# Optimization experiments

Measured on AMD Instinct MI355X. Metric: run time of the kernel, lower is better.

The kernel has to match this reference:

```python
import jax, jax.numpy as jnp
import numpy as np

D_MODEL = 1024
N_HEADS = 16
D_K = D_MODEL // N_HEADS


def setup_inputs() -> dict:
    key = jax.random.key(0)
    ks = jax.random.split(key, 11)
    B, S = 2, 2048
    s = 1.0 / np.sqrt(D_MODEL)
    return {
        "Q": jax.random.normal(ks[0], (B, S, D_MODEL), jnp.float32),
        "K": jax.random.normal(ks[1], (B, S, D_MODEL), jnp.float32),
        "V": jax.random.normal(ks[2], (B, S, D_MODEL), jnp.float32),
        "Wq": jax.random.normal(ks[3], (D_MODEL, D_MODEL), jnp.float32) * s,
        "bq": jnp.zeros((D_MODEL,), jnp.float32),
        "Wk": jax.random.normal(ks[4], (D_MODEL, D_MODEL), jnp.float32) * s,
        "bk": jnp.zeros((D_MODEL,), jnp.float32),
        "Wv": jax.random.normal(ks[5], (D_MODEL, D_MODEL), jnp.float32) * s,
        "bv": jnp.zeros((D_MODEL,), jnp.float32),
        "Wo": jax.random.normal(ks[6], (D_MODEL, D_MODEL), jnp.float32) * s,
        "bo": jnp.zeros((D_MODEL,), jnp.float32),
    }


def reference(Q, K, V, Wq, bq, Wk, bk, Wv, bv, Wo, bo):
    B, S, _ = Q.shape
    # linear projections (torch Linear: x @ W.T + b), split into heads
    def proj(x, W, b):
        y = x @ W.T + b                          # [B,S,D]
        return y.reshape(B, -1, N_HEADS, D_K).transpose(0, 2, 1, 3)  # [B,H,S,d_k]
    q = proj(Q, Wq, bq)
    k = proj(K, Wk, bk)
    v = proj(V, Wv, bv)
    scale = 1.0 / jnp.sqrt(jnp.float32(D_K))
    scores = jnp.einsum('bhqd,bhkd->bhqk', q, k) * scale  # [B,H,S,S]
    attn = jax.nn.softmax(scores, axis=-1)
    out = jnp.einsum('bhqk,bhkd->bhqd', attn, v)          # [B,H,S,d_k]
    out = out.transpose(0, 2, 1, 3).reshape(B, S, N_HEADS * D_K)
    return out @ Wo.T + bo
```

## Files before the change

### kernel.cpp

```cpp
#include <hip/hip_runtime.h>
#include <hip/hip_bf16.h>
#include <math.h>

#define D_MODEL 1024
#define NH      16
#define DK      64
#define S_LEN   2048
#define BATCH   2
#define M_ROWS  4096

typedef _Float16 f16;
typedef _Float16 f16x8 __attribute__((ext_vector_type(8)));
typedef float    f32x4 __attribute__((ext_vector_type(4)));

__device__ __forceinline__ float exp2_fast(float x) {
    float r;
    asm("v_exp_f32 %0, %1" : "=v"(r) : "v"(x));
    return r;
}

__device__ __forceinline__ int perm6(int k) {
    return (k & 35) | ((k & 12) << 1) | ((k & 16) >> 2);
}

__global__ __launch_bounds__(256) void cvt_f32_to_f16(
    const float* __restrict__ a, const float* __restrict__ b,
    const float* __restrict__ c, const float* __restrict__ d,
    f16* __restrict__ oa, f16* __restrict__ ob,
    f16* __restrict__ oc, f16* __restrict__ od, int n8) {
    const int y = blockIdx.y;
    const float* s = (y == 0) ? a : (y == 1) ? b : (y == 2) ? c : d;
    f16* o        = (y == 0) ? oa : (y == 1) ? ob : (y == 2) ? oc : od;
    if (s == nullptr) return;
    const int i = blockIdx.x * 256 + threadIdx.x;
    if (i >= n8) return;
    const size_t e = (size_t)i * 8;
    const float4 v0 = *(const float4*)&s[e];
    const float4 v1 = *(const float4*)&s[e + 4];
    f16x8 r = {(f16)v0.x, (f16)v0.y, (f16)v0.z, (f16)v0.w,
               (f16)v1.x, (f16)v1.y, (f16)v1.z, (f16)v1.w};
    *(f16x8*)&o[e] = r;
}

__device__ __forceinline__ void stage16(const f16* g, f16* l) {
    __builtin_amdgcn_global_load_lds(
        (const __attribute__((address_space(1))) unsigned int*)g,
        (__attribute__((address_space(3))) unsigned int*)l, 16, 0, 0);
}

__device__ __forceinline__ void gemm_body(f16* As, f16* Bs,
                                          const f16* __restrict__ X, const f16* __restrict__ W,
                                          const float* __restrict__ bias, void* __restrict__ Yv,
                                          const int mode, const float oscale) {
    const int tid = threadIdx.x;
    const int lane = tid & 63;
    const int w  = tid >> 6;
    const int wm = w >> 1, wn = w & 1;
    const int l15 = lane & 15, lhi = lane >> 4;
    const int m0 = blockIdx.y * 128, n0 = blockIdx.x * 128;

    const int srow = tid >> 2;
    const int scol = (tid & 3) * 8;

    f32x4 acc[4][4] = {};

    for (int k0 = 0; k0 < D_MODEL; k0 += 32) {
        __syncthreads();
        stage16(&X[(size_t)(m0 + srow) * D_MODEL + k0 + scol],      &As[tid * 8]);
        stage16(&X[(size_t)(m0 + 64 + srow) * D_MODEL + k0 + scol], &As[2048 + tid * 8]);
        stage16(&W[(size_t)(n0 + srow) * D_MODEL + k0 + scol],      &Bs[tid * 8]);
        stage16(&W[(size_t)(n0 + 64 + srow) * D_MODEL + k0 + scol], &Bs[2048 + tid * 8]);
        __syncthreads();
        f16x8 af[4], bf[4];
#pragma unroll
        for (int mt = 0; mt < 4; ++mt) af[mt] = *(const f16x8*)&As[(wm * 64 + mt * 16 + l15) * 32 + lhi * 8];
#pragma unroll
        for (int nt = 0; nt < 4; ++nt) bf[nt] = *(const f16x8*)&Bs[(wn * 64 + nt * 16 + l15) * 32 + lhi * 8];
#pragma unroll
        for (int mt = 0; mt < 4; ++mt)
#pragma unroll
            for (int nt = 0; nt < 4; ++nt)
                acc[mt][nt] = __builtin_amdgcn_mfma_f32_16x16x32_f16(af[mt], bf[nt], acc[mt][nt], 0, 0, 0);
    }

#pragma unroll
    for (int mt = 0; mt < 4; ++mt)
#pragma unroll
        for (int nt = 0; nt < 4; ++nt) {
            const int n = n0 + wn * 64 + nt * 16 + l15;
            const float bn = bias[n];
#pragma unroll
            for (int r = 0; r < 4; ++r) {
                const int m = m0 + wm * 64 + mt * 16 + lhi * 4 + r;
                const float v = (acc[mt][nt][r] + bn) * oscale;
                if (mode == 0) {
                    ((f16*)Yv)[((((size_t)(m >> 11) * NH + (n >> 6)) * S_LEN) + (m & 2047)) * DK + (n & 63)] = (f16)v;
                } else {
                    ((float*)Yv)[(size_t)m * D_MODEL + n] = v;
                }
            }
        }
}

__device__ __forceinline__ void gemm_body_vswap(f16* As, f16* Bs,
                                                const f16* __restrict__ X, const f16* __restrict__ W,
                                                const float* __restrict__ bias, f16* __restrict__ vt) {
    const int tid = threadIdx.x;
    const int lane = tid & 63;
    const int w  = tid >> 6;
    const int wm = w >> 1, wn = w & 1;
    const int l15 = lane & 15, lhi = lane >> 4;
    const int m0 = blockIdx.y * 128, n0 = blockIdx.x * 128;

    const int srow = tid >> 2;
    const int scol = (tid & 3) * 8;

    f32x4 acc[4][4] = {};

    for (int k0 = 0; k0 < D_MODEL; k0 += 32) {
        __syncthreads();
        stage16(&X[(size_t)(m0 + srow) * D_MODEL + k0 + scol],      &As[tid * 8]);
        stage16(&X[(size_t)(m0 + 64 + srow) * D_MODEL + k0 + scol], &As[2048 + tid * 8]);
        stage16(&W[(size_t)(n0 + srow) * D_MODEL + k0 + scol],      &Bs[tid * 8]);
        stage16(&W[(size_t)(n0 + 64 + srow) * D_MODEL + k0 + scol], &Bs[2048 + tid * 8]);
        __syncthreads();
        f16x8 af[4], bf[4];
#pragma unroll
        for (int at = 0; at < 4; ++at) af[at] = *(const f16x8*)&Bs[(wm * 64 + at * 16 + l15) * 32 + lhi * 8];
#pragma unroll
        for (int bt = 0; bt < 4; ++bt) bf[bt] = *(const f16x8*)&As[(wn * 64 + bt * 16 + l15) * 32 + lhi * 8];
#pragma unroll
        for (int at = 0; at < 4; ++at)
#pragma unroll
            for (int bt = 0; bt < 4; ++bt)
                acc[at][bt] = __builtin_amdgcn_mfma_f32_16x16x32_f16(af[at], bf[bt], acc[at][bt], 0, 0, 0);
    }

#pragma unroll
    for (int at = 0; at < 4; ++at)
#pragma unroll
        for (int bt = 0; bt < 4; ++bt) {
            const int m = m0 + wn * 64 + bt * 16 + l15;
            const int b = m >> 11, s = m & 2047;
#pragma unroll
            for (int r = 0; r < 4; ++r) {
                const int n = n0 + wm * 64 + at * 16 + lhi * 4 + r;
                const float v = acc[at][bt][r] + bias[n];
                const int s2 = (s & ~63) | perm6(s & 63);
                vt[(((size_t)b * NH + (n >> 6)) * DK + (n & 63)) * S_LEN + s2] = (f16)v;
            }
        }
}

__global__ __launch_bounds__(256) void qkv_gemm(
    const f16* __restrict__ Xq, const f16* __restrict__ Xk, const f16* __restrict__ Xv,
    const f16* __restrict__ Wq, const f16* __restrict__ Wk, const f16* __restrict__ Wv,
    const float* __restrict__ bq, const float* __restrict__ bk, const float* __restrict__ bv,
    f16* __restrict__ qh, f16* __restrict__ kh, f16* __restrict__ vt) {
    __shared__ f16 As[128 * 32];
    __shared__ f16 Bs[128 * 32];
    const int z = blockIdx.z;
    if (z == 2) {
        gemm_body_vswap(As, Bs, Xv, Wv, bv, vt);
    } else if (z == 0) {
        gemm_body(As, Bs, Xq, Wq, bq, qh, 0, 0.125f * 1.44269504f);
    } else {
        gemm_body(As, Bs, Xk, Wk, bk, kh, 0, 1.0f);
    }
}

__global__ __launch_bounds__(256) void out_gemm(const f16* __restrict__ X, const f16* __restrict__ W,
                                                const float* __restrict__ bias, float* __restrict__ Y) {
    __shared__ f16 As[64 * 32];
    __shared__ f16 Bs[128 * 32];
    const int tid = threadIdx.x;
    const int lane = tid & 63;
    const int w  = tid >> 6;
    const int l15 = lane & 15, lhi = lane >> 4;
    const int m0 = blockIdx.y * 64, n0 = blockIdx.x * 128;

    const int srow = tid >> 2;
    const int scol = (tid & 3) * 8;

    f32x4 acc[4][2] = {};

    for (int k0 = 0; k0 < D_MODEL; k0 += 32) {
        __syncthreads();
        stage16(&X[(size_t)(m0 + srow) * D_MODEL + k0 + scol],      &As[tid * 8]);
        stage16(&W[(size_t)(n0 + srow) * D_MODEL + k0 + scol],      &Bs[tid * 8]);
        stage16(&W[(size_t)(n0 + 64 + srow) * D_MODEL + k0 + scol], &Bs[2048 + tid * 8]);
        __syncthreads();
        f16x8 af[4], bf[2];
#pragma unroll
        for (int mt = 0; mt < 4; ++mt) af[mt] = *(const f16x8*)&As[(mt * 16 + l15) * 32 + lhi * 8];
#pragma unroll
        for (int nt = 0; nt < 2; ++nt) bf[nt] = *(const f16x8*)&Bs[(w * 32 + nt * 16 + l15) * 32 + lhi * 8];
#pragma unroll
        for (int mt = 0; mt < 4; ++mt)
#pragma unroll
            for (int nt = 0; nt < 2; ++nt)
                acc[mt][nt] = __builtin_amdgcn_mfma_f32_16x16x32_f16(af[mt], bf[nt], acc[mt][nt], 0, 0, 0);
    }

#pragma unroll
    for (int mt = 0; mt < 4; ++mt)
#pragma unroll
        for (int nt = 0; nt < 2; ++nt) {
            const int n = n0 + w * 32 + nt * 16 + l15;
            const float bn = bias[n];
#pragma unroll
            for (int r = 0; r < 4; ++r) {
                const int m = m0 + mt * 16 + lhi * 4 + r;
                Y[(size_t)m * D_MODEL + n] = acc[mt][nt][r] + bn;
            }
        }
}

__global__ __launch_bounds__(256) void flash_mfma(const f16* __restrict__ qh, const f16* __restrict__ kh,
                                                  const f16* __restrict__ vt, f16* __restrict__ ao) {
    __shared__ f16 Ks[64][72];
    __shared__ f16 Vs[64][72];

    const int tid = threadIdx.x;
    const int lane = tid & 63;
    const int w = tid >> 6;
    const int c = lane & 15;
    const int g = lane >> 4;
    const int qt = blockIdx.x, bh = blockIdx.y;
    const int b = bh >> 4, h = bh & 15;
    const int qrow0 = qt * 64 + w * 16;

    f16x8 bQ0, bQ1;
    {
        const f16* qp = qh + ((size_t)bh * S_LEN + qrow0 + c) * DK;
        bQ0 = *(const f16x8*)&qp[g * 8];
        bQ1 = *(const f16x8*)&qp[32 + g * 8];
    }

    f32x4 oa[4] = {};
    float m_run = -INFINITY;
    float l_run = 0.f;

    const int cr = tid >> 3;
    const int cs = (tid & 7) * 8;

    const f16* kbase = kh + (size_t)bh * S_LEN * DK;
    const f16* vbase = vt + (size_t)bh * DK * S_LEN;

    uint4 kA = *(const uint4*)&kbase[(size_t)(cr) * DK + cs];
    uint4 kB = *(const uint4*)&kbase[(size_t)(cr + 32) * DK + cs];
    uint4 vA = *(const uint4*)&vbase[(size_t)cr * S_LEN + cs];
    uint4 vB = *(const uint4*)&vbase[(size_t)(cr + 32) * S_LEN + cs];

    for (int kt = 0; kt < S_LEN / 64; ++kt) {
        __syncthreads();
        *(uint4*)&Ks[cr][cs]      = kA;
        *(uint4*)&Ks[cr + 32][cs] = kB;
        *(uint4*)&Vs[cr][cs]      = vA;
        *(uint4*)&Vs[cr + 32][cs] = vB;
        if (kt + 1 < S_LEN / 64) {
            const int o = (kt + 1) * 64;
            kA = *(const uint4*)&kbase[(size_t)(o + cr) * DK + cs];
            kB = *(const uint4*)&kbase[(size_t)(o + cr + 32) * DK + cs];
            vA = *(const uint4*)&vbase[(size_t)cr * S_LEN + o + cs];
            vB = *(const uint4*)&vbase[(size_t)(cr + 32) * S_LEN + o + cs];
        }
        __syncthreads();

        f32x4 sc[4] = {};
        __builtin_amdgcn_s_setprio(1);
#pragma unroll
        for (int nt = 0; nt < 4; ++nt) {
            const f16x8 ka = *(const f16x8*)&Ks[nt * 16 + c][g * 8];
            const f16x8 kb = *(const f16x8*)&Ks[nt * 16 + c][32 + g * 8];
            sc[nt] = __builtin_amdgcn_mfma_f32_16x16x32_f16(ka, bQ0, sc[nt], 0, 0, 0);
            sc[nt] = __builtin_amdgcn_mfma_f32_16x16x32_f16(kb, bQ1, sc[nt], 0, 0, 0);
        }
        __builtin_amdgcn_s_setprio(0);

        float tmax = sc[0][0];
#pragma unroll
        for (int nt = 0; nt < 4; ++nt)
#pragma unroll
            for (int r = 0; r < 4; ++r) tmax = fmaxf(tmax, sc[nt][r]);
        tmax = fmaxf(tmax, __shfl_xor(tmax, 16));
        tmax = fmaxf(tmax, __shfl_xor(tmax, 32));

        if (!__all(tmax <= m_run + 8.f)) {
            const float mnew = fmaxf(m_run, tmax);
            const float fac = exp2_fast(m_run - mnew);
            m_run = mnew;
            l_run *= fac;
#pragma unroll
            for (int r = 0; r < 4; ++r) {
                const float fr = __shfl(fac, (lane & 48) + ((lane >> 4) & 3) * 4 + r);
                oa[0][r] *= fr; oa[1][r] *= fr; oa[2][r] *= fr; oa[3][r] *= fr;
            }
        }

        float e[4][4];
        float tsum = 0.f;
#pragma unroll
        for (int nt = 0; nt < 4; ++nt)
#pragma unroll
            for (int r = 0; r < 4; ++r) {
                e[nt][r] = exp2_fast(sc[nt][r] - m_run);
                tsum += e[nt][r];
            }
        tsum += __shfl_xor(tsum, 16);
        tsum += __shfl_xor(tsum, 32);
        l_run += tsum;

        const f16x8 aP0 = {(f16)e[0][0], (f16)e[0][1], (f16)e[0][2], (f16)e[0][3],
                           (f16)e[1][0], (f16)e[1][1], (f16)e[1][2], (f16)e[1][3]};
        const f16x8 aP1 = {(f16)e[2][0], (f16)e[2][1], (f16)e[2][2], (f16)e[2][3],
                           (f16)e[3][0], (f16)e[3][1], (f16)e[3][2], (f16)e[3][3]};

        __builtin_amdgcn_s_setprio(1);
#pragma unroll
        for (int nt2 = 0; nt2 < 4; ++nt2) {
            const f16x8 b0 = *(const f16x8*)&Vs[nt2 * 16 + c][g * 8];
            const f16x8 b1 = *(const f16x8*)&Vs[nt2 * 16 + c][32 + g * 8];
            oa[nt2] = __builtin_amdgcn_mfma_f32_16x16x32_f16(aP0, b0, oa[nt2], 0, 0, 0);
            oa[nt2] = __builtin_amdgcn_mfma_f32_16x16x32_f16(aP1, b1, oa[nt2], 0, 0, 0);
        }
        __builtin_amdgcn_s_setprio(0);
    }

    const float invc = 1.f / l_run;
#pragma unroll
    for (int r = 0; r < 4; ++r) {
        const float ir = __shfl(invc, (lane & 48) + ((lane >> 4) & 3) * 4 + r);
        const int srow = qrow0 + ((lane >> 4) & 3) * 4 + r;
#pragma unroll
        for (int nt2 = 0; nt2 < 4; ++nt2) {
            ao[((size_t)b * S_LEN + srow) * D_MODEL + h * DK + nt2 * 16 + c] = (f16)(oa[nt2][r] * ir);
        }
    }
}

extern "C" void kernel_launch(void* const* d_in, const int* in_sizes, int n_in,
                              void* d_out, int out_size, void* d_ws, size_t ws_size,
                              hipStream_t stream) {
    const float* Q  = (const float*)d_in[0];
    const float* K  = (const float*)d_in[1];
    const float* V  = (const float*)d_in[2];
    const float* Wq = (const float*)d_in[3];
    const float* bq = (const float*)d_in[4];
    const float* Wk = (const float*)d_in[5];
    const float* bk = (const float*)d_in[6];
    const float* Wv = (const float*)d_in[7];
    const float* bv = (const float*)d_in[8];
    const float* Wo = (const float*)d_in[9];
    const float* bo = (const float*)d_in[10];
    float* out = (float*)d_out;

    const size_t NELEM = (size_t)M_ROWS * D_MODEL;
    const size_t WELEM = (size_t)D_MODEL * D_MODEL;
    f16* Qf  = (f16*)d_ws;
    f16* Kf  = Qf + NELEM;
    f16* Vf  = Kf + NELEM;
    f16* Wqf = Vf + NELEM;
    f16* Wkf = Wqf + WELEM;
    f16* Wvf = Wkf + WELEM;
    f16* Wof = Wvf + WELEM;
    f16* qh  = Wof + WELEM;
    f16* kh  = qh + NELEM;
    f16* vtw = kh + NELEM;
    f16* aow = vtw + NELEM;

    cvt_f32_to_f16<<<dim3(2048, 3), 256, 0, stream>>>(Q, K, V, nullptr, Qf, Kf, Vf, nullptr,
                                                      (int)(NELEM / 8));
    cvt_f32_to_f16<<<dim3(512, 4), 256, 0, stream>>>(Wq, Wk, Wv, Wo, Wqf, Wkf, Wvf, Wof,
                                                     (int)(WELEM / 8));
    qkv_gemm<<<dim3(D_MODEL / 128, M_ROWS / 128, 3), 256, 0, stream>>>(
        Qf, Kf, Vf, Wqf, Wkf, Wvf, bq, bk, bv, qh, kh, vtw);
    flash_mfma<<<dim3(S_LEN / 64, BATCH * NH), 256, 0, stream>>>(qh, kh, vtw, aow);
    out_gemm<<<dim3(D_MODEL / 128, M_ROWS / 64), 256, 0, stream>>>(aow, Wof, bo, out);
}
```

Before: 251.5 us.

## Load K/V fragments directly into registers and process two query subtiles per wave

```diff
diff --git a/kernel.cpp b/kernel.cpp
--- a/kernel.cpp
+++ b/kernel.cpp
@@ -218,123 +218,130 @@
 
 __global__ __launch_bounds__(256) void flash_mfma(const f16* __restrict__ qh, const f16* __restrict__ kh,
                                                   const f16* __restrict__ vt, f16* __restrict__ ao) {
-    __shared__ f16 Ks[64][72];
-    __shared__ f16 Vs[64][72];
-
     const int tid = threadIdx.x;
     const int lane = tid & 63;
     const int w = tid >> 6;
-    const int c = lane & 15;
-    const int g = lane >> 4;
-    const int qt = blockIdx.x, bh = blockIdx.y;
+    const int c = lane & 15, g = lane >> 4;
+    const int bid = blockIdx.x;
+    const int swz = (bid & 7) * 64 + (bid >> 3);
+    const int bh = swz >> 4, qt = swz & 15;
     const int b = bh >> 4, h = bh & 15;
-    const int qrow0 = qt * 64 + w * 16;
-
-    f16x8 bQ0, bQ1;
-    {
-        const f16* qp = qh + ((size_t)bh * S_LEN + qrow0 + c) * DK;
-        bQ0 = *(const f16x8*)&qp[g * 8];
-        bQ1 = *(const f16x8*)&qp[32 + g * 8];
-    }
-
-    f32x4 oa[4] = {};
-    float m_run = -INFINITY;
-    float l_run = 0.f;
-
-    const int cr = tid >> 3;
-    const int cs = (tid & 7) * 8;
+    const int qbase = qt * 128 + w * 32;
 
     const f16* kbase = kh + (size_t)bh * S_LEN * DK;
     const f16* vbase = vt + (size_t)bh * DK * S_LEN;
 
-    uint4 kA = *(const uint4*)&kbase[(size_t)(cr) * DK + cs];
-    uint4 kB = *(const uint4*)&kbase[(size_t)(cr + 32) * DK + cs];
-    uint4 vA = *(const uint4*)&vbase[(size_t)cr * S_LEN + cs];
-    uint4 vB = *(const uint4*)&vbase[(size_t)(cr + 32) * S_LEN + cs];
+    f16x8 bQ[2][2];
+#pragma unroll
+    for (int s = 0; s < 2; ++s) {
+        const f16* qp = qh + ((size_t)bh * S_LEN + qbase + s * 16 + c) * DK;
+        bQ[s][0] = *(const f16x8*)&qp[g * 8];
+        bQ[s][1] = *(const f16x8*)&qp[32 + g * 8];
+    }
+
+    f32x4 oa[2][4] = {};
+    float m_run[2] = {-INFINITY, -INFINITY};
+    float l_run[2] = {0.f, 0.f};
+
+    f16x8 kf[8];
+#pragma unroll
+    for (int nt = 0; nt < 4; ++nt) {
+        const f16* kp = &kbase[(size_t)(nt * 16 + c) * DK];
+        kf[nt * 2]     = *(const f16x8*)&kp[g * 8];
+        kf[nt * 2 + 1] = *(const f16x8*)&kp[32 + g * 8];
+    }
 
     for (int kt = 0; kt < S_LEN / 64; ++kt) {
-        __syncthreads();
-        *(uint4*)&Ks[cr][cs]      = kA;
-        *(uint4*)&Ks[cr + 32][cs] = kB;
-        *(uint4*)&Vs[cr][cs]      = vA;
-        *(uint4*)&Vs[cr + 32][cs] = vB;
+        f16x8 vf[8];
+#pragma unroll
+        for (int nt2 = 0; nt2 < 4; ++nt2) {
+            const f16* vp = &vbase[(size_t)(nt2 * 16 + c) * S_LEN + kt * 64];
+            vf[nt2 * 2]     = *(const f16x8*)&vp[g * 8];
+            vf[nt2 * 2 + 1] = *(const f16x8*)&vp[32 + g * 8];
+        }
+
+        f32x4 sc[2][4] = {};
+        __builtin_amdgcn_s_setprio(1);
+#pragma unroll
+        for (int nt = 0; nt < 4; ++nt) {
+#pragma unroll
+            for (int s = 0; s < 2; ++s) {
+                sc[s][nt] = __builtin_amdgcn_mfma_f32_16x16x32_f16(kf[nt * 2],     bQ[s][0], sc[s][nt], 0, 0, 0);
+                sc[s][nt] = __builtin_amdgcn_mfma_f32_16x16x32_f16(kf[nt * 2 + 1], bQ[s][1], sc[s][nt], 0, 0, 0);
+            }
+        }
+        __builtin_amdgcn_s_setprio(0);
+
         if (kt + 1 < S_LEN / 64) {
-            const int o = (kt + 1) * 64;
-            kA = *(const uint4*)&kbase[(size_t)(o + cr) * DK + cs];
-            kB = *(const uint4*)&kbase[(size_t)(o + cr + 32) * DK + cs];
-            vA = *(const uint4*)&vbase[(size_t)cr * S_LEN + o + cs];
-            vB = *(const uint4*)&vbase[(size_t)(cr + 32) * S_LEN + o + cs];
-        }
-        __syncthreads();
-
-        f32x4 sc[4] = {};
-        __builtin_amdgcn_s_setprio(1);
-#pragma unroll
-        for (int nt = 0; nt < 4; ++nt) {
-            const f16x8 ka = *(const f16x8*)&Ks[nt * 16 + c][g * 8];
-            const f16x8 kb = *(const f16x8*)&Ks[nt * 16 + c][32 + g * 8];
-            sc[nt] = __builtin_amdgcn_mfma_f32_16x16x32_f16(ka, bQ0, sc[nt], 0, 0, 0);
-            sc[nt] = __builtin_amdgcn_mfma_f32_16x16x32_f16(kb, bQ1, sc[nt], 0, 0, 0);
-        }
-        __builtin_amdgcn_s_setprio(0);
-
-        float tmax = sc[0][0];
-#pragma unroll
-        for (int nt = 0; nt < 4; ++nt)
-#pragma unroll
-            for (int r = 0; r < 4; ++r) tmax = fmaxf(tmax, sc[nt][r]);
-        tmax = fmaxf(tmax, __shfl_xor(tmax, 16));
-        tmax = fmaxf(tmax, __shfl_xor(tmax, 32));
-
-        if (!__all(tmax <= m_run + 8.f)) {
-            const float mnew = fmaxf(m_run, tmax);
-            const float fac = exp2_fast(m_run - mnew);
-            m_run = mnew;
-            l_run *= fac;
-#pragma unroll
-            for (int r = 0; r < 4; ++r) {
-                const float fr = __shfl(fac, (lane & 48) + ((lane >> 4) & 3) * 4 + r);
-                oa[0][r] *= fr; oa[1][r] *= fr; oa[2][r] *= fr; oa[3][r] *= fr;
-            }
-        }
-
-        float e[4][4];
-        float tsum = 0.f;
-#pragma unroll
-        for (int nt = 0; nt < 4; ++nt)
-#pragma unroll
-            for (int r = 0; r < 4; ++r) {
-                e[nt][r] = exp2_fast(sc[nt][r] - m_run);
-                tsum += e[nt][r];
-            }
-        tsum += __shfl_xor(tsum, 16);
-        tsum += __shfl_xor(tsum, 32);
-        l_run += tsum;
-
-        const f16x8 aP0 = {(f16)e[0][0], (f16)e[0][1], (f16)e[0][2], (f16)e[0][3],
-                           (f16)e[1][0], (f16)e[1][1], (f16)e[1][2], (f16)e[1][3]};
-        const f16x8 aP1 = {(f16)e[2][0], (f16)e[2][1], (f16)e[2][2], (f16)e[2][3],
-                           (f16)e[3][0], (f16)e[3][1], (f16)e[3][2], (f16)e[3][3]};
-
-        __builtin_amdgcn_s_setprio(1);
-#pragma unroll
-        for (int nt2 = 0; nt2 < 4; ++nt2) {
-            const f16x8 b0 = *(const f16x8*)&Vs[nt2 * 16 + c][g * 8];
-            const f16x8 b1 = *(const f16x8*)&Vs[nt2 * 16 + c][32 + g * 8];
-            oa[nt2] = __builtin_amdgcn_mfma_f32_16x16x32_f16(aP0, b0, oa[nt2], 0, 0, 0);
-            oa[nt2] = __builtin_amdgcn_mfma_f32_16x16x32_f16(aP1, b1, oa[nt2], 0, 0, 0);
-        }
-        __builtin_amdgcn_s_setprio(0);
-    }
-
-    const float invc = 1.f / l_run;
-#pragma unroll
-    for (int r = 0; r < 4; ++r) {
-        const float ir = __shfl(invc, (lane & 48) + ((lane >> 4) & 3) * 4 + r);
-        const int srow = qrow0 + ((lane >> 4) & 3) * 4 + r;
-#pragma unroll
-        for (int nt2 = 0; nt2 < 4; ++nt2) {
-            ao[((size_t)b * S_LEN + srow) * D_MODEL + h * DK + nt2 * 16 + c] = (f16)(oa[nt2][r] * ir);
+#pragma unroll
+            for (int nt = 0; nt < 4; ++nt) {
+                const f16* kp = &kbase[(size_t)((kt + 1) * 64 + nt * 16 + c) * DK];
+                kf[nt * 2]     = *(const f16x8*)&kp[g * 8];
+                kf[nt * 2 + 1] = *(const f16x8*)&kp[32 + g * 8];
+            }
+        }
+
+#pragma unroll
+        for (int s = 0; s < 2; ++s) {
+            float tmax = sc[s][0][0];
+#pragma unroll
+            for (int nt = 0; nt < 4; ++nt)
+#pragma unroll
+                for (int r = 0; r < 4; ++r) tmax = fmaxf(tmax, sc[s][nt][r]);
+            tmax = fmaxf(tmax, __shfl_xor(tmax, 16));
+            tmax = fmaxf(tmax, __shfl_xor(tmax, 32));
+
+            if (!__all(tmax <= m_run[s] + 8.f)) {
+                const float mnew = fmaxf(m_run[s], tmax);
+                const float fac = exp2_fast(m_run[s] - mnew);
+                m_run[s] = mnew;
+                l_run[s] *= fac;
+#pragma unroll
+                for (int r = 0; r < 4; ++r) {
+                    const float fr = __shfl(fac, (lane & 48) + ((lane >> 4) & 3) * 4 + r);
+                    oa[s][0][r] *= fr; oa[s][1][r] *= fr; oa[s][2][r] *= fr; oa[s][3][r] *= fr;
+                }
+            }
+
+            float e[4][4];
+            float tsum = 0.f;
+#pragma unroll
+            for (int nt = 0; nt < 4; ++nt)
+#pragma unroll
+                for (int r = 0; r < 4; ++r) {
+                    e[nt][r] = exp2_fast(sc[s][nt][r] - m_run[s]);
+                    tsum += e[nt][r];
+                }
+            tsum += __shfl_xor(tsum, 16);
+            tsum += __shfl_xor(tsum, 32);
+            l_run[s] += tsum;
+
+            const f16x8 aP0 = {(f16)e[0][0], (f16)e[0][1], (f16)e[0][2], (f16)e[0][3],
+                               (f16)e[1][0], (f16)e[1][1], (f16)e[1][2], (f16)e[1][3]};
+            const f16x8 aP1 = {(f16)e[2][0], (f16)e[2][1], (f16)e[2][2], (f16)e[2][3],
+                               (f16)e[3][0], (f16)e[3][1], (f16)e[3][2], (f16)e[3][3]};
+
+            __builtin_amdgcn_s_setprio(1);
+#pragma unroll
+            for (int nt2 = 0; nt2 < 4; ++nt2) {
+                oa[s][nt2] = __builtin_amdgcn_mfma_f32_16x16x32_f16(aP0, vf[nt2 * 2],     oa[s][nt2], 0, 0, 0);
+                oa[s][nt2] = __builtin_amdgcn_mfma_f32_16x16x32_f16(aP1, vf[nt2 * 2 + 1], oa[s][nt2], 0, 0, 0);
+            }
+            __builtin_amdgcn_s_setprio(0);
+        }
+    }
+
+#pragma unroll
+    for (int s = 0; s < 2; ++s) {
+        const float invc = 1.f / l_run[s];
+#pragma unroll
+        for (int r = 0; r < 4; ++r) {
+            const float ir = __shfl(invc, (lane & 48) + ((lane >> 4) & 3) * 4 + r);
+            const int srow = qbase + s * 16 + g * 4 + r;
+#pragma unroll
+            for (int nt2 = 0; nt2 < 4; ++nt2) {
+                ao[((size_t)b * S_LEN + srow) * D_MODEL + h * DK + nt2 * 16 + c] = (f16)(oa[s][nt2][r] * ir);
+            }
         }
     }
 }
@@ -375,6 +382,6 @@
                                                      (int)(WELEM / 8));
     qkv_gemm<<<dim3(D_MODEL / 128, M_ROWS / 128, 3), 256, 0, stream>>>(
         Qf, Kf, Vf, Wqf, Wkf, Wvf, bq, bk, bv, qh, kh, vtw);
-    flash_mfma<<<dim3(S_LEN / 64, BATCH * NH), 256, 0, stream>>>(qh, kh, vtw, aow);
+    flash_mfma<<<512, 256, 0, stream>>>(qh, kh, vtw, aow);
     out_gemm<<<dim3(D_MODEL / 128, M_ROWS / 64), 256, 0, stream>>>(aow, Wof, bo, out);
 }
```

After: 304.9 us. 21.2% more time.

## Merge conversion launches and stage two K/V tiles per barrier in flash kernel

Applied to the files above, without the earlier changes.

```diff
diff --git a/kernel.cpp b/kernel.cpp
--- a/kernel.cpp
+++ b/kernel.cpp
@@ -23,15 +23,19 @@
     return (k & 35) | ((k & 12) << 1) | ((k & 16) >> 2);
 }
 
-__global__ __launch_bounds__(256) void cvt_f32_to_f16(
-    const float* __restrict__ a, const float* __restrict__ b,
-    const float* __restrict__ c, const float* __restrict__ d,
-    f16* __restrict__ oa, f16* __restrict__ ob,
-    f16* __restrict__ oc, f16* __restrict__ od, int n8) {
+__global__ __launch_bounds__(256) void cvt7(
+    const float* __restrict__ s0, const float* __restrict__ s1, const float* __restrict__ s2,
+    const float* __restrict__ s3, const float* __restrict__ s4, const float* __restrict__ s5,
+    const float* __restrict__ s6,
+    f16* __restrict__ d0, f16* __restrict__ d1, f16* __restrict__ d2,
+    f16* __restrict__ d3, f16* __restrict__ d4, f16* __restrict__ d5,
+    f16* __restrict__ d6, int n8big, int n8small) {
     const int y = blockIdx.y;
-    const float* s = (y == 0) ? a : (y == 1) ? b : (y == 2) ? c : d;
-    f16* o        = (y == 0) ? oa : (y == 1) ? ob : (y == 2) ? oc : od;
-    if (s == nullptr) return;
+    const float* s = (y == 0) ? s0 : (y == 1) ? s1 : (y == 2) ? s2 : (y == 3) ? s3
+                   : (y == 4) ? s4 : (y == 5) ? s5 : s6;
+    f16* d        = (y == 0) ? d0 : (y == 1) ? d1 : (y == 2) ? d2 : (y == 3) ? d3
+                   : (y == 4) ? d4 : (y == 5) ? d5 : d6;
+    const int n8 = (y < 3) ? n8big : n8small;
     const int i = blockIdx.x * 256 + threadIdx.x;
     if (i >= n8) return;
     const size_t e = (size_t)i * 8;
@@ -39,7 +43,7 @@
     const float4 v1 = *(const float4*)&s[e + 4];
     f16x8 r = {(f16)v0.x, (f16)v0.y, (f16)v0.z, (f16)v0.w,
                (f16)v1.x, (f16)v1.y, (f16)v1.z, (f16)v1.w};
-    *(f16x8*)&o[e] = r;
+    *(f16x8*)&d[e] = r;
 }
 
 __device__ __forceinline__ void stage16(const f16* g, f16* l) {
@@ -218,8 +222,8 @@
 
 __global__ __launch_bounds__(256) void flash_mfma(const f16* __restrict__ qh, const f16* __restrict__ kh,
                                                   const f16* __restrict__ vt, f16* __restrict__ ao) {
-    __shared__ f16 Ks[64][72];
-    __shared__ f16 Vs[64][72];
+    __shared__ f16 Ks[2][64][72];
+    __shared__ f16 Vs[2][64][72];
 
     const int tid = threadIdx.x;
     const int lane = tid & 63;
@@ -247,84 +251,97 @@
     const f16* kbase = kh + (size_t)bh * S_LEN * DK;
     const f16* vbase = vt + (size_t)bh * DK * S_LEN;
 
-    uint4 kA = *(const uint4*)&kbase[(size_t)(cr) * DK + cs];
-    uint4 kB = *(const uint4*)&kbase[(size_t)(cr + 32) * DK + cs];
-    uint4 vA = *(const uint4*)&vbase[(size_t)cr * S_LEN + cs];
-    uint4 vB = *(const uint4*)&vbase[(size_t)(cr + 32) * S_LEN + cs];
-
-    for (int kt = 0; kt < S_LEN / 64; ++kt) {
-        __syncthreads();
-        *(uint4*)&Ks[cr][cs]      = kA;
-        *(uint4*)&Ks[cr + 32][cs] = kB;
-        *(uint4*)&Vs[cr][cs]      = vA;
-        *(uint4*)&Vs[cr + 32][cs] = vB;
-        if (kt + 1 < S_LEN / 64) {
-            const int o = (kt + 1) * 64;
-            kA = *(const uint4*)&kbase[(size_t)(o + cr) * DK + cs];
-            kB = *(const uint4*)&kbase[(size_t)(o + cr + 32) * DK + cs];
-            vA = *(const uint4*)&vbase[(size_t)cr * S_LEN + o + cs];
-            vB = *(const uint4*)&vbase[(size_t)(cr + 32) * S_LEN + o + cs];
-        }
-        __syncthreads();
-
-        f32x4 sc[4] = {};
-        __builtin_amdgcn_s_setprio(1);
-#pragma unroll
-        for (int nt = 0; nt < 4; ++nt) {
-            const f16x8 ka = *(const f16x8*)&Ks[nt * 16 + c][g * 8];
-            const f16x8 kb = *(const f16x8*)&Ks[nt * 16 + c][32 + g * 8];
-            sc[nt] = __builtin_amdgcn_mfma_f32_16x16x32_f16(ka, bQ0, sc[nt], 0, 0, 0);
-            sc[nt] = __builtin_amdgcn_mfma_f32_16x16x32_f16(kb, bQ1, sc[nt], 0, 0, 0);
-        }
-        __builtin_amdgcn_s_setprio(0);
-
-        float tmax = sc[0][0];
-#pragma unroll
-        for (int nt = 0; nt < 4; ++nt)
-#pragma unroll
-            for (int r = 0; r < 4; ++r) tmax = fmaxf(tmax, sc[nt][r]);
-        tmax = fmaxf(tmax, __shfl_xor(tmax, 16));
-        tmax = fmaxf(tmax, __shfl_xor(tmax, 32));
-
-        if (!__all(tmax <= m_run + 8.f)) {
-            const float mnew = fmaxf(m_run, tmax);
-            const float fac = exp2_fast(m_run - mnew);
-            m_run = mnew;
-            l_run *= fac;
-#pragma unroll
-            for (int r = 0; r < 4; ++r) {
-                const float fr = __shfl(fac, (lane & 48) + ((lane >> 4) & 3) * 4 + r);
-                oa[0][r] *= fr; oa[1][r] *= fr; oa[2][r] *= fr; oa[3][r] *= fr;
-            }
-        }
-
-        float e[4][4];
-        float tsum = 0.f;
-#pragma unroll
-        for (int nt = 0; nt < 4; ++nt)
-#pragma unroll
-            for (int r = 0; r < 4; ++r) {
-                e[nt][r] = exp2_fast(sc[nt][r] - m_run);
-                tsum += e[nt][r];
-            }
-        tsum += __shfl_xor(tsum, 16);
-        tsum += __shfl_xor(tsum, 32);
-        l_run += tsum;
-
-        const f16x8 aP0 = {(f16)e[0][0], (f16)e[0][1], (f16)e[0][2], (f16)e[0][3],
-                           (f16)e[1][0], (f16)e[1][1], (f16)e[1][2], (f16)e[1][3]};
-        const f16x8 aP1 = {(f16)e[2][0], (f16)e[2][1], (f16)e[2][2], (f16)e[2][3],
-                           (f16)e[3][0], (f16)e[3][1], (f16)e[3][2], (f16)e[3][3]};
-
-        __builtin_amdgcn_s_setprio(1);
-#pragma unroll
-        for (int nt2 = 0; nt2 < 4; ++nt2) {
-            const f16x8 b0 = *(const f16x8*)&Vs[nt2 * 16 + c][g * 8];
-            const f16x8 b1 = *(const f16x8*)&Vs[nt2 * 16 + c][32 + g * 8];
-            oa[nt2] = __builtin_amdgcn_mfma_f32_16x16x32_f16(aP0, b0, oa[nt2], 0, 0, 0);
-            oa[nt2] = __builtin_amdgcn_mfma_f32_16x16x32_f16(aP1, b1, oa[nt2], 0, 0, 0);
-        }
-        __builtin_amdgcn_s_setprio(0);
+    uint4 kr[2][2], vr[2][2];
+#pragma unroll
+    for (int s = 0; s < 2; ++s) {
+        kr[s][0] = *(const uint4*)&kbase[(size_t)(s * 64 + cr) * DK + cs];
+        kr[s][1] = *(const uint4*)&kbase[(size_t)(s * 64 + cr + 32) * DK + cs];
+        vr[s][0] = *(const uint4*)&vbase[(size_t)cr * S_LEN + s * 64 + cs];
+        vr[s][1] = *(const uint4*)&vbase[(size_t)(cr + 32) * S_LEN + s * 64 + cs];
+    }
+
+    for (int bt = 0; bt < S_LEN / 128; ++bt) {
+        __syncthreads();
+#pragma unroll
+        for (int s = 0; s < 2; ++s) {
+            *(uint4*)&Ks[s][cr][cs]      = kr[s][0];
+            *(uint4*)&Ks[s][cr + 32][cs] = kr[s][1];
+            *(uint4*)&Vs[s][cr][cs]      = vr[s][0];
+            *(uint4*)&Vs[s][cr + 32][cs] = vr[s][1];
+        }
+        if (bt + 1 < S_LEN / 128) {
+            const int o = (bt + 1) * 128;
+#pragma unroll
+            for (int s = 0; s < 2; ++s) {
+                kr[s][0] = *(const uint4*)&kbase[(size_t)(o + s * 64 + cr) * DK + cs];
+                kr[s][1] = *(const uint4*)&kbase[(size_t)(o + s * 64 + cr + 32) * DK + cs];
+                vr[s][0] = *(const uint4*)&vbase[(size_t)cr * S_LEN + o + s * 64 + cs];
+                vr[s][1] = *(const uint4*)&vbase[(size_t)(cr + 32) * S_LEN + o + s * 64 + cs];
+            }
+        }
+        __syncthreads();
+
+#pragma unroll
+        for (int sub = 0; sub < 2; ++sub) {
+            f32x4 sc[4] = {};
+            __builtin_amdgcn_s_setprio(1);
+#pragma unroll
+            for (int nt = 0; nt < 4; ++nt) {
+                const f16x8 ka = *(const f16x8*)&Ks[sub][nt * 16 + c][g * 8];
+                const f16x8 kb = *(const f16x8*)&Ks[sub][nt * 16 + c][32 + g * 8];
+                sc[nt] = __builtin_amdgcn_mfma_f32_16x16x32_f16(ka, bQ0, sc[nt], 0, 0, 0);
+                sc[nt] = __builtin_amdgcn_mfma_f32_16x16x32_f16(kb, bQ1, sc[nt], 0, 0, 0);
+            }
+            __builtin_amdgcn_s_setprio(0);
+
+            float tmax = sc[0][0];
+#pragma unroll
+            for (int nt = 0; nt < 4; ++nt)
+#pragma unroll
+                for (int r = 0; r < 4; ++r) tmax = fmaxf(tmax, sc[nt][r]);
+            tmax = fmaxf(tmax, __shfl_xor(tmax, 16));
+            tmax = fmaxf(tmax, __shfl_xor(tmax, 32));
+
+            if (!__all(tmax <= m_run + 8.f)) {
+                const float mnew = fmaxf(m_run, tmax);
+                const float fac = exp2_fast(m_run - mnew);
+                m_run = mnew;
+                l_run *= fac;
+#pragma unroll
+                for (int r = 0; r < 4; ++r) {
+                    const float fr = __shfl(fac, (lane & 48) + ((lane >> 4) & 3) * 4 + r);
+                    oa[0][r] *= fr; oa[1][r] *= fr; oa[2][r] *= fr; oa[3][r] *= fr;
+                }
+            }
+
+            float e[4][4];
+            float tsum = 0.f;
+#pragma unroll
+            for (int nt = 0; nt < 4; ++nt)
+#pragma unroll
+                for (int r = 0; r < 4; ++r) {
+                    e[nt][r] = exp2_fast(sc[nt][r] - m_run);
+                    tsum += e[nt][r];
+                }
+            tsum += __shfl_xor(tsum, 16);
+            tsum += __shfl_xor(tsum, 32);
+            l_run += tsum;
+
+            const f16x8 aP0 = {(f16)e[0][0], (f16)e[0][1], (f16)e[0][2], (f16)e[0][3],
+                               (f16)e[1][0], (f16)e[1][1], (f16)e[1][2], (f16)e[1][3]};
+            const f16x8 aP1 = {(f16)e[2][0], (f16)e[2][1], (f16)e[2][2], (f16)e[2][3],
+                               (f16)e[3][0], (f16)e[3][1], (f16)e[3][2], (f16)e[3][3]};
+
+            __builtin_amdgcn_s_setprio(1);
+#pragma unroll
+            for (int nt2 = 0; nt2 < 4; ++nt2) {
+                const f16x8 b0 = *(const f16x8*)&Vs[sub][nt2 * 16 + c][g * 8];
+                const f16x8 b1 = *(const f16x8*)&Vs[sub][nt2 * 16 + c][32 + g * 8];
+                oa[nt2] = __builtin_amdgcn_mfma_f32_16x16x32_f16(aP0, b0, oa[nt2], 0, 0, 0);
+                oa[nt2] = __builtin_amdgcn_mfma_f32_16x16x32_f16(aP1, b1, oa[nt2], 0, 0, 0);
+            }
+            __builtin_amdgcn_s_setprio(0);
+        }
     }
 
     const float invc = 1.f / l_run;
@@ -369,10 +386,9 @@
     f16* vtw = kh + NELEM;
     f16* aow = vtw + NELEM;
 
-    cvt_f32_to_f16<<<dim3(2048, 3), 256, 0, stream>>>(Q, K, V, nullptr, Qf, Kf, Vf, nullptr,
-                                                      (int)(NELEM / 8));
-    cvt_f32_to_f16<<<dim3(512, 4), 256, 0, stream>>>(Wq, Wk, Wv, Wo, Wqf, Wkf, Wvf, Wof,
-                                                     (int)(WELEM / 8));
+    cvt7<<<dim3(2048, 7), 256, 0, stream>>>(Q, K, V, Wq, Wk, Wv, Wo,
+                                            Qf, Kf, Vf, Wqf, Wkf, Wvf, Wof,
+                                            (int)(NELEM / 8), (int)(WELEM / 8));
     qkv_gemm<<<dim3(D_MODEL / 128, M_ROWS / 128, 3), 256, 0, stream>>>(
         Qf, Kf, Vf, Wqf, Wkf, Wvf, bq, bk, bv, qh, kh, vtw);
     flash_mfma<<<dim3(S_LEN / 64, BATCH * NH), 256, 0, stream>>>(qh, kh, vtw, aow);
```

After: 347.9 us. 38.3% more time.

## Stage QKV GEMM epilogue through LDS for coalesced stores; merge conversion launches

Applied to the files above, without the earlier changes.

```diff
diff --git a/kernel.cpp b/kernel.cpp
--- a/kernel.cpp
+++ b/kernel.cpp
@@ -23,15 +23,19 @@
     return (k & 35) | ((k & 12) << 1) | ((k & 16) >> 2);
 }
 
-__global__ __launch_bounds__(256) void cvt_f32_to_f16(
-    const float* __restrict__ a, const float* __restrict__ b,
-    const float* __restrict__ c, const float* __restrict__ d,
-    f16* __restrict__ oa, f16* __restrict__ ob,
-    f16* __restrict__ oc, f16* __restrict__ od, int n8) {
+__global__ __launch_bounds__(256) void cvt7(
+    const float* __restrict__ s0, const float* __restrict__ s1, const float* __restrict__ s2,
+    const float* __restrict__ s3, const float* __restrict__ s4, const float* __restrict__ s5,
+    const float* __restrict__ s6,
+    f16* __restrict__ d0, f16* __restrict__ d1, f16* __restrict__ d2,
+    f16* __restrict__ d3, f16* __restrict__ d4, f16* __restrict__ d5,
+    f16* __restrict__ d6, int n8big, int n8small) {
     const int y = blockIdx.y;
-    const float* s = (y == 0) ? a : (y == 1) ? b : (y == 2) ? c : d;
-    f16* o        = (y == 0) ? oa : (y == 1) ? ob : (y == 2) ? oc : od;
-    if (s == nullptr) return;
+    const float* s = (y == 0) ? s0 : (y == 1) ? s1 : (y == 2) ? s2 : (y == 3) ? s3
+                   : (y == 4) ? s4 : (y == 5) ? s5 : s6;
+    f16* d        = (y == 0) ? d0 : (y == 1) ? d1 : (y == 2) ? d2 : (y == 3) ? d3
+                   : (y == 4) ? d4 : (y == 5) ? d5 : d6;
+    const int n8 = (y < 3) ? n8big : n8small;
     const int i = blockIdx.x * 256 + threadIdx.x;
     if (i >= n8) return;
     const size_t e = (size_t)i * 8;
@@ -39,7 +43,7 @@
     const float4 v1 = *(const float4*)&s[e + 4];
     f16x8 r = {(f16)v0.x, (f16)v0.y, (f16)v0.z, (f16)v0.w,
                (f16)v1.x, (f16)v1.y, (f16)v1.z, (f16)v1.w};
-    *(f16x8*)&o[e] = r;
+    *(f16x8*)&d[e] = r;
 }
 
 __device__ __forceinline__ void stage16(const f16* g, f16* l) {
@@ -83,23 +87,55 @@
                 acc[mt][nt] = __builtin_amdgcn_mfma_f32_16x16x32_f16(af[mt], bf[nt], acc[mt][nt], 0, 0, 0);
     }
 
-#pragma unroll
-    for (int mt = 0; mt < 4; ++mt)
-#pragma unroll
-        for (int nt = 0; nt < 4; ++nt) {
-            const int n = n0 + wn * 64 + nt * 16 + l15;
-            const float bn = bias[n];
-#pragma unroll
-            for (int r = 0; r < 4; ++r) {
-                const int m = m0 + wm * 64 + mt * 16 + lhi * 4 + r;
-                const float v = (acc[mt][nt][r] + bn) * oscale;
-                if (mode == 0) {
-                    ((f16*)Yv)[((((size_t)(m >> 11) * NH + (n >> 6)) * S_LEN) + (m & 2047)) * DK + (n & 63)] = (f16)v;
-                } else {
-                    ((float*)Yv)[(size_t)m * D_MODEL + n] = v;
+    if (mode == 2) {
+#pragma unroll
+        for (int mt = 0; mt < 4; ++mt)
+#pragma unroll
+            for (int nt = 0; nt < 4; ++nt) {
+                const int n = n0 + wn * 64 + nt * 16 + l15;
+                const float bn = bias[n];
+#pragma unroll
+                for (int r = 0; r < 4; ++r) {
+                    const int m = m0 + wm * 64 + mt * 16 + lhi * 4 + r;
+                    ((float*)Yv)[(size_t)m * D_MODEL + n] = (acc[mt][nt][r] + bn) * oscale;
                 }
             }
-        }
+        return;
+    }
+
+    f16* pool = (w & 1) ? Bs : As;
+    const int myphase = w >> 1;
+#pragma unroll
+    for (int phase = 0; phase < 2; ++phase) {
+        __syncthreads();
+        if (myphase == phase) {
+#pragma unroll
+            for (int nt = 0; nt < 4; ++nt) {
+                const int n = n0 + wn * 64 + nt * 16 + l15;
+                const float bn = bias[n];
+#pragma unroll
+                for (int mt = 0; mt < 4; ++mt)
+#pragma unroll
+                    for (int r = 0; r < 4; ++r)
+                        pool[(mt * 16 + lhi * 4 + r) * 64 + nt * 16 + l15] =
+                            (f16)((acc[mt][nt][r] + bn) * oscale);
+        }
+        }
+        __syncthreads();
+        if (myphase == phase) {
+            const int nbase = n0 + wn * 64;
+            const int h = nbase >> 6;
+            const int col = (lane & 7) * 8;
+#pragma unroll
+            for (int t = 0; t < 8; ++t) {
+                const int row = t * 8 + (lane >> 3);
+                const int m = m0 + wm * 64 + row;
+                const int b = m >> 11, s = m & 2047;
+                const f16x8 v = *(const f16x8*)&pool[row * 64 + col];
+                *(f16x8*)&((f16*)Yv)[((((size_t)b * NH + h) * S_LEN) + s) * DK + col] = v;
+            }
+        }
+    }
 }
 
 __device__ __forceinline__ void gemm_body_vswap(f16* As, f16* Bs,
@@ -136,20 +172,38 @@
                 acc[at][bt] = __builtin_amdgcn_mfma_f32_16x16x32_f16(af[at], bf[bt], acc[at][bt], 0, 0, 0);
     }
 
-#pragma unroll
-    for (int at = 0; at < 4; ++at)
-#pragma unroll
-        for (int bt = 0; bt < 4; ++bt) {
-            const int m = m0 + wn * 64 + bt * 16 + l15;
-            const int b = m >> 11, s = m & 2047;
-#pragma unroll
-            for (int r = 0; r < 4; ++r) {
-                const int n = n0 + wm * 64 + at * 16 + lhi * 4 + r;
-                const float v = acc[at][bt][r] + bias[n];
-                const int s2 = (s & ~63) | perm6(s & 63);
-                vt[(((size_t)b * NH + (n >> 6)) * DK + (n & 63)) * S_LEN + s2] = (f16)v;
-            }
-        }
+    f16* pool = (w & 1) ? Bs : As;
+    const int myphase = w >> 1;
+#pragma unroll
+    for (int phase = 0; phase < 2; ++phase) {
+        __syncthreads();
+        if (myphase == phase) {
+#pragma unroll
+            for (int at = 0; at < 4; ++at)
+#pragma unroll
+                for (int r = 0; r < 4; ++r) {
+                    const int nl = at * 16 + lhi * 4 + r;
+                    const float bn = bias[n0 + wm * 64 + nl];
+#pragma unroll
+                    for (int bt = 0; bt < 4; ++bt)
+                        pool[nl * 64 + perm6(bt * 16 + l15)] = (f16)(acc[at][bt][r] + bn);
+                }
+        }
+        __syncthreads();
+        if (myphase == phase) {
+            const int nbase = n0 + wm * 64;
+            const int h = nbase >> 6;
+            const int mbase = m0 + wn * 64;
+            const int b = mbase >> 11, sblk = mbase & 2047;
+            const int col = (lane & 7) * 8;
+#pragma unroll
+            for (int t = 0; t < 8; ++t) {
+                const int row = t * 8 + (lane >> 3);
+                const f16x8 v = *(const f16x8*)&pool[row * 64 + col];
+                *(f16x8*)&vt[(((size_t)b * NH + h) * DK + row) * S_LEN + sblk + col] = v;
+            }
+        }
+    }
 }
 
 __global__ __launch_bounds__(256) void qkv_gemm(
@@ -369,10 +423,9 @@
     f16* vtw = kh + NELEM;
     f16* aow = vtw + NELEM;
 
-    cvt_f32_to_f16<<<dim3(2048, 3), 256, 0, stream>>>(Q, K, V, nullptr, Qf, Kf, Vf, nullptr,
-                                                      (int)(NELEM / 8));
-    cvt_f32_to_f16<<<dim3(512, 4), 256, 0, stream>>>(Wq, Wk, Wv, Wo, Wqf, Wkf, Wvf, Wof,
-                                                     (int)(WELEM / 8));
+    cvt7<<<dim3(2048, 7), 256, 0, stream>>>(Q, K, V, Wq, Wk, Wv, Wo,
+                                            Qf, Kf, Vf, Wqf, Wkf, Wvf, Wof,
+                                            (int)(NELEM / 8), (int)(WELEM / 8));
     qkv_gemm<<<dim3(D_MODEL / 128, M_ROWS / 128, 3), 256, 0, stream>>>(
         Qf, Kf, Vf, Wqf, Wkf, Wvf, bq, bk, bv, qh, kh, vtw);
     flash_mfma<<<dim3(S_LEN / 64, BATCH * NH), 256, 0, stream>>>(qh, kh, vtw, aow);
```

New measurement: 254.0 us. Within noise of the previous version (+1.0%).
